# Performance work log

Hardware: AMD Instinct MI355X
Metric: run time of the kernel (lower is better)

## Reference

```python
import jax, jax.numpy as jnp
import numpy as np

T = 64        # n_estimators
DEPTH = 8
D = 2**DEPTH - 1   # internal nodes per tree (255)
K = 2**DEPTH       # leaves per tree (256)
M = 512       # n_features
C = 8         # class_num
B = 4096      # batch


def _build_path_masks():
    # Complete binary tree in heap order. For leaf l, walk from root;
    # going LEFT corresponds to b==+1 -> multiply (1 - x_node) -> Bpos,
    # going RIGHT corresponds to b==-1 -> multiply x_node -> Bneg.
    Bpos = np.zeros((K, D), dtype=np.float32)
    Bneg = np.zeros((K, D), dtype=np.float32)
    for l in range(K):
        node = 0
        for level in range(DEPTH):
            bit = (l >> (DEPTH - 1 - level)) & 1
            if bit == 0:
                Bpos[l, node] = 1.0
            else:
                Bneg[l, node] = 1.0
            node = 2 * node + 1 + bit
    return Bpos, Bneg


def setup_inputs() -> dict:
    rng = np.random.default_rng(0)
    key = jax.random.key(0)
    x = jax.random.normal(key, (B, M), dtype=jnp.float32)
    # fcn1: each internal node splits on one feature -> one-hot weight row,
    # bias = -threshold (change_parameters1).
    feat = rng.integers(0, M, size=(T, D))
    W1 = np.zeros((T, D, M), dtype=np.float32)
    W1[np.arange(T)[:, None], np.arange(D)[None, :], feat] = 1.0
    b1 = (-rng.standard_normal((T, D))).astype(np.float32)  # -threshold
    # Path masks shared across trees (complete trees), tiled per tree.
    Bpos1, Bneg1 = _build_path_masks()
    Bpos = np.broadcast_to(Bpos1, (T, K, D)).copy()
    Bneg = np.broadcast_to(Bneg1, (T, K, D)).copy()
    # fcn2 weight = c^T with zero bias (change_parameters2): leaf values [T, K, C]
    Cw = rng.random((T, K, C)).astype(np.float32)
    return {
        "input": x,
        "W1": jnp.asarray(W1),
        "b1": jnp.asarray(b1),
        "Bpos": jnp.asarray(Bpos),
        "Bneg": jnp.asarray(Bneg),
        "Cw": jnp.asarray(Cw),
    }


def reference(input, W1, b1, Bpos, Bneg, Cw):
    # z: [B, T, D] = 10 * (fcn1 per tree)
    z = 10.0 * (jnp.einsum("bm,tdm->btd", input, W1) + b1)
    # x = sigmoid(z); leaf-path product:
    #   x_c[b,t,k] = prod_d x^Bneg[t,k,d] * (1-x)^Bpos[t,k,d]
    # computed exactly in log-space (all factors in (0,1)):
    log_x = jax.nn.log_sigmoid(z)       # log sigmoid(z)
    log_1mx = jax.nn.log_sigmoid(-z)    # log (1 - sigmoid(z))
    log_xc = (jnp.einsum("btd,tkd->btk", log_x, Bneg)
              + jnp.einsum("btd,tkd->btk", log_1mx, Bpos))
    x_c = jnp.exp(log_xc)               # [B, T, K]
    # fcn2 (zero bias) then forest average over trees
    out = jnp.einsum("btk,tkc->bc", x_c, Cw) / T
    return out
```

## Files before the change

kernel.cpp:

```cpp
#include <hip/hip_runtime.h>
#include <hip/hip_bf16.h>

#define TT 64
#define DD 255
#define KK 256
#define MM 512
#define CC 8
#define BB 4096
#define NB 4

typedef _Float16 h2 __attribute__((ext_vector_type(2)));

__device__ __forceinline__ float wave_sum(float v) {
    v += __shfl_down(v, 32, 64);
    v += __shfl_down(v, 16, 64);
    v += __shfl_down(v, 8, 64);
    v += __shfl_down(v, 4, 64);
    v += __shfl_down(v, 2, 64);
    v += __shfl_down(v, 1, 64);
    return v;
}

__global__ void feat_kernel(const float* __restrict__ W1, int* __restrict__ feat) {
    const int row = blockIdx.x * 4 + (threadIdx.x >> 6);
    const int lane = threadIdx.x & 63;
    const float4* r = reinterpret_cast<const float4*>(W1 + (size_t)row * MM);
    float4 a = r[lane];
    float4 b = r[lane + 64];
    float ba = (float)(4 * lane);
    float bb = (float)(4 * (lane + 64));
    float acc = 0.0f;
    acc = fmaf(a.x, ba,        acc);
    acc = fmaf(a.y, ba + 1.0f, acc);
    acc = fmaf(a.z, ba + 2.0f, acc);
    acc = fmaf(a.w, ba + 3.0f, acc);
    acc = fmaf(b.x, bb,        acc);
    acc = fmaf(b.y, bb + 1.0f, acc);
    acc = fmaf(b.z, bb + 2.0f, acc);
    acc = fmaf(b.w, bb + 3.0f, acc);
    acc = wave_sum(acc);
    if (lane == 0) feat[row] = (int)(acc + 0.5f);
}

__device__ __forceinline__ float sigm_from(float xv, float c1) {
    float earg = fmaf(-14.426950408889634f, xv, c1);
    float e = exp2f(earg);
    return __builtin_amdgcn_rcpf(1.0f + e);
}

#define FMA4(acc, s, v)                         \
    do {                                        \
        (acc).x = fmaf((s), (v).x, (acc).x);    \
        (acc).y = fmaf((s), (v).y, (acc).y);    \
        (acc).z = fmaf((s), (v).z, (acc).z);    \
        (acc).w = fmaf((s), (v).w, (acc).w);    \
    } while (0)

__global__ __launch_bounds__(256, 4) void forest_kernel(
        const float* __restrict__ x, const float* __restrict__ b1,
        const float* __restrict__ Cw, const int* __restrict__ feat,
        float* __restrict__ out) {
    __shared__ float xsi[MM][NB];
    __shared__ h2 s8[NB * 2 * 256 * 2];
    __shared__ float4 red4[4][NB][2];

    const int tid = threadIdx.x;
    const int b0 = blockIdx.x * NB;

    for (int idx = tid; idx < MM * NB; idx += 256) {
        int m = idx & (MM - 1);
        int bl = idx >> 9;
        xsi[m][bl] = x[(size_t)(b0 + bl) * MM + m];
    }

    float4 accA[NB], accB[NB];
    #pragma unroll
    for (int bl = 0; bl < NB; ++bl) {
        accA[bl] = make_float4(0.f, 0.f, 0.f, 0.f);
        accB[bl] = make_float4(0.f, 0.f, 0.f, 0.f);
    }

    const int i = tid & 127;
    const int sub = tid >> 7;

    for (int g = 0; g < 8; ++g) {
        __syncthreads();
        if (tid < DD) {
            const int d = tid;
            int f[8];
            float c1[8];
            #pragma unroll
            for (int j = 0; j < 8; ++j) {
                int t = g * 8 + j;
                f[j] = feat[t * DD + d];
                c1[j] = -14.426950408889634f * b1[t * DD + d];
            }
            float sv[NB][8];
            #pragma unroll
            for (int j = 0; j < 8; ++j) {
                float4 xv = *reinterpret_cast<const float4*>(&xsi[f[j]][0]);
                sv[0][j] = sigm_from(xv.x, c1[j]);
                sv[1][j] = sigm_from(xv.y, c1[j]);
                sv[2][j] = sigm_from(xv.z, c1[j]);
                sv[3][j] = sigm_from(xv.w, c1[j]);
            }
            #pragma unroll
            for (int bl = 0; bl < NB; ++bl) {
                h2 p0 = {(_Float16)sv[bl][0], (_Float16)sv[bl][1]};
                h2 p1 = {(_Float16)sv[bl][2], (_Float16)sv[bl][3]};
                h2 p2 = {(_Float16)sv[bl][4], (_Float16)sv[bl][5]};
                h2 p3 = {(_Float16)sv[bl][6], (_Float16)sv[bl][7]};
                float2 w0, w1;
                w0.x = __builtin_bit_cast(float, p0);
                w0.y = __builtin_bit_cast(float, p1);
                w1.x = __builtin_bit_cast(float, p2);
                w1.y = __builtin_bit_cast(float, p3);
                *reinterpret_cast<float2*>(&s8[(bl * 2 + 0) * 512 + d * 2]) = w0;
                *reinterpret_cast<float2*>(&s8[(bl * 2 + 1) * 512 + d * 2]) = w1;
            }
        }
        __syncthreads();

        float4 cA0[4], cA1[4], cB0[4], cB1[4];
        #pragma unroll
        for (int j = 0; j < 4; ++j) {
            int t = g * 8 + sub * 4 + j;
            const float4* p = reinterpret_cast<const float4*>(
                Cw + ((size_t)t * KK + 2 * i) * CC);
            cA0[j] = p[0];
            cA1[j] = p[1];
            cB0[j] = p[2];
            cB1[j] = p[3];
        }

        h2 pre0[NB], pre1[NB];
        #pragma unroll
        for (int bl = 0; bl < NB; ++bl) {
            pre0[bl] = (h2){(_Float16)1.0f, (_Float16)1.0f};
            pre1[bl] = (h2){(_Float16)1.0f, (_Float16)1.0f};
        }

        #pragma unroll
        for (int lev = 0; lev < 7; ++lev) {
            int node = (1 << lev) - 1 + (i >> (7 - lev));
            int bit = (i >> (6 - lev)) & 1;
            _Float16 offs = (_Float16)(1 - bit);
            _Float16 sgs = (_Float16)(2 * bit - 1);
            h2 offv = {offs, offs};
            h2 sg = {sgs, sgs};
            #pragma unroll
            for (int bl = 0; bl < NB; ++bl) {
                float2 raw = *reinterpret_cast<const float2*>(
                    &s8[(bl * 2 + sub) * 512 + node * 2]);
                h2 s0 = __builtin_bit_cast(h2, raw.x);
                h2 s1 = __builtin_bit_cast(h2, raw.y);
                pre0[bl] *= (sg * s0 + offv);
                pre1[bl] *= (sg * s1 + offv);
            }
        }
        const int node7 = 127 + i;
        #pragma unroll
        for (int bl = 0; bl < NB; ++bl) {
            float2 raw = *reinterpret_cast<const float2*>(
                &s8[(bl * 2 + sub) * 512 + node7 * 2]);
            h2 s0 = __builtin_bit_cast(h2, raw.x);
            h2 s1 = __builtin_bit_cast(h2, raw.y);
            h2 one = {(_Float16)1.0f, (_Float16)1.0f};
            h2 pe0h = pre0[bl] * (one - s0);
            h2 po0h = pre0[bl] * s0;
            h2 pe1h = pre1[bl] * (one - s1);
            h2 po1h = pre1[bl] * s1;
            float pear[4] = {(float)pe0h.x, (float)pe0h.y,
                             (float)pe1h.x, (float)pe1h.y};
            float poar[4] = {(float)po0h.x, (float)po0h.y,
                             (float)po1h.x, (float)po1h.y};
            #pragma unroll
            for (int j = 0; j < 4; ++j) {
                FMA4(accA[bl], pear[j], cA0[j]);
                FMA4(accB[bl], pear[j], cA1[j]);
                FMA4(accA[bl], poar[j], cB0[j]);
                FMA4(accB[bl], poar[j], cB1[j]);
            }
        }
    }

    const int lane = tid & 63;
    const int wv = tid >> 6;
    #pragma unroll
    for (int bl = 0; bl < NB; ++bl) {
        accA[bl].x = wave_sum(accA[bl].x);
        accA[bl].y = wave_sum(accA[bl].y);
        accA[bl].z = wave_sum(accA[bl].z);
        accA[bl].w = wave_sum(accA[bl].w);
        accB[bl].x = wave_sum(accB[bl].x);
        accB[bl].y = wave_sum(accB[bl].y);
        accB[bl].z = wave_sum(accB[bl].z);
        accB[bl].w = wave_sum(accB[bl].w);
    }
    if (lane == 0) {
        #pragma unroll
        for (int bl = 0; bl < NB; ++bl) {
            red4[wv][bl][0] = accA[bl];
            red4[wv][bl][1] = accB[bl];
        }
    }
    __syncthreads();
    if (tid < NB * CC) {
        int bl = tid >> 3;
        int c = tid & 7;
        const float* r0 = reinterpret_cast<const float*>(&red4[0][bl][0]);
        const float* r1 = reinterpret_cast<const float*>(&red4[1][bl][0]);
        const float* r2 = reinterpret_cast<const float*>(&red4[2][bl][0]);
        const float* r3 = reinterpret_cast<const float*>(&red4[3][bl][0]);
        float s = r0[c] + r1[c] + r2[c] + r3[c];
        out[(size_t)(b0 + bl) * CC + c] = s * (1.0f / 64.0f);
    }
}

extern "C" void kernel_launch(void* const* d_in, const int* in_sizes, int n_in,
                              void* d_out, int out_size, void* d_ws, size_t ws_size,
                              hipStream_t stream) {
    const float* x  = (const float*)d_in[0];
    const float* W1 = (const float*)d_in[1];
    const float* b1 = (const float*)d_in[2];
    const float* Cw = (const float*)d_in[5];
    float* out = (float*)d_out;
    int* feat = (int*)d_ws;

    feat_kernel<<<(TT * DD) / 4, 256, 0, stream>>>(W1, feat);
    forest_kernel<<<BB / NB, 256, 0, stream>>>(x, b1, Cw, feat, out);
}
```

Baseline: 169.4 us.

## Use packed fp16 leaf accumulation and split trees across two grid halves

Replaces the fp32 FMA accumulation of leaf probability times class weight with packed half2 multiply-adds, converting Cw to fp16 in registers. The tree loop is split over a second grid dimension (two halves of 32 trees), and partial sums are combined with atomicAdd after a memset of the output. This roughly halves the ALU work of the reduction and doubles the block count for better occupancy. The cost is fp16 accumulation error, a duplicated x load per half, and atomics.

New measurement: 167.6 us. About the same (-1.0%).

```diff
diff --git a/kernel.cpp b/kernel.cpp
--- a/kernel.cpp
+++ b/kernel.cpp
@@ -8,6 +8,7 @@
 #define CC 8
 #define BB 4096
 #define NB 4
+#define TPB 32
 
 typedef _Float16 h2 __attribute__((ext_vector_type(2)));
 
@@ -48,24 +49,17 @@
     return __builtin_amdgcn_rcpf(1.0f + e);
 }
 
-#define FMA4(acc, s, v)                         \
-    do {                                        \
-        (acc).x = fmaf((s), (v).x, (acc).x);    \
-        (acc).y = fmaf((s), (v).y, (acc).y);    \
-        (acc).z = fmaf((s), (v).z, (acc).z);    \
-        (acc).w = fmaf((s), (v).w, (acc).w);    \
-    } while (0)
-
-__global__ __launch_bounds__(256, 4) void forest_kernel(
+__global__ __launch_bounds__(256, 2) void forest_kernel(
         const float* __restrict__ x, const float* __restrict__ b1,
         const float* __restrict__ Cw, const int* __restrict__ feat,
         float* __restrict__ out) {
     __shared__ float xsi[MM][NB];
     __shared__ h2 s8[NB * 2 * 256 * 2];
-    __shared__ float4 red4[4][NB][2];
+    __shared__ float red[4][NB][CC];
 
     const int tid = threadIdx.x;
     const int b0 = blockIdx.x * NB;
+    const int t0 = blockIdx.y * TPB;
 
     for (int idx = tid; idx < MM * NB; idx += 256) {
         int m = idx & (MM - 1);
@@ -73,17 +67,18 @@
         xsi[m][bl] = x[(size_t)(b0 + bl) * MM + m];
     }
 
-    float4 accA[NB], accB[NB];
+    h2 acc[NB][4];
     #pragma unroll
-    for (int bl = 0; bl < NB; ++bl) {
-        accA[bl] = make_float4(0.f, 0.f, 0.f, 0.f);
-        accB[bl] = make_float4(0.f, 0.f, 0.f, 0.f);
-    }
+    for (int bl = 0; bl < NB; ++bl)
+        #pragma unroll
+        for (int q = 0; q < 4; ++q)
+            acc[bl][q] = (h2){(_Float16)0.0f, (_Float16)0.0f};
 
     const int i = tid & 127;
     const int sub = tid >> 7;
-
-    for (int g = 0; g < 8; ++g) {
+    const h2 one = {(_Float16)1.0f, (_Float16)1.0f};
+
+    for (int g = 0; g < TPB / 8; ++g) {
         __syncthreads();
         if (tid < DD) {
             const int d = tid;
@@ -91,7 +86,7 @@
             float c1[8];
             #pragma unroll
             for (int j = 0; j < 8; ++j) {
-                int t = g * 8 + j;
+                int t = t0 + g * 8 + j;
                 f[j] = feat[t * DD + d];
                 c1[j] = -14.426950408889634f * b1[t * DD + d];
             }
@@ -121,23 +116,28 @@
         }
         __syncthreads();
 
-        float4 cA0[4], cA1[4], cB0[4], cB1[4];
+        h2 cwa[4][4], cwb[4][4];
         #pragma unroll
         for (int j = 0; j < 4; ++j) {
-            int t = g * 8 + sub * 4 + j;
+            int t = t0 + g * 8 + sub * 4 + j;
             const float4* p = reinterpret_cast<const float4*>(
                 Cw + ((size_t)t * KK + 2 * i) * CC);
-            cA0[j] = p[0];
-            cA1[j] = p[1];
-            cB0[j] = p[2];
-            cB1[j] = p[3];
+            float4 a0 = p[0], a1 = p[1], bv0 = p[2], bv1 = p[3];
+            cwa[j][0] = (h2){(_Float16)a0.x, (_Float16)a0.y};
+            cwa[j][1] = (h2){(_Float16)a0.z, (_Float16)a0.w};
+            cwa[j][2] = (h2){(_Float16)a1.x, (_Float16)a1.y};
+            cwa[j][3] = (h2){(_Float16)a1.z, (_Float16)a1.w};
+            cwb[j][0] = (h2){(_Float16)bv0.x, (_Float16)bv0.y};
+            cwb[j][1] = (h2){(_Float16)bv0.z, (_Float16)bv0.w};
+            cwb[j][2] = (h2){(_Float16)bv1.x, (_Float16)bv1.y};
+            cwb[j][3] = (h2){(_Float16)bv1.z, (_Float16)bv1.w};
         }
 
         h2 pre0[NB], pre1[NB];
         #pragma unroll
         for (int bl = 0; bl < NB; ++bl) {
-            pre0[bl] = (h2){(_Float16)1.0f, (_Float16)1.0f};
-            pre1[bl] = (h2){(_Float16)1.0f, (_Float16)1.0f};
+            pre0[bl] = one;
+            pre1[bl] = one;
         }
 
         #pragma unroll
@@ -165,55 +165,48 @@
                 &s8[(bl * 2 + sub) * 512 + node7 * 2]);
             h2 s0 = __builtin_bit_cast(h2, raw.x);
             h2 s1 = __builtin_bit_cast(h2, raw.y);
-            h2 one = {(_Float16)1.0f, (_Float16)1.0f};
-            h2 pe0h = pre0[bl] * (one - s0);
-            h2 po0h = pre0[bl] * s0;
-            h2 pe1h = pre1[bl] * (one - s1);
-            h2 po1h = pre1[bl] * s1;
-            float pear[4] = {(float)pe0h.x, (float)pe0h.y,
-                             (float)pe1h.x, (float)pe1h.y};
-            float poar[4] = {(float)po0h.x, (float)po0h.y,
-                             (float)po1h.x, (float)po1h.y};
-            #pragma unroll
-            for (int j = 0; j < 4; ++j) {
-                FMA4(accA[bl], pear[j], cA0[j]);
-                FMA4(accB[bl], pear[j], cA1[j]);
-                FMA4(accA[bl], poar[j], cB0[j]);
-                FMA4(accB[bl], poar[j], cB1[j]);
+            h2 pe0 = pre0[bl] * (one - s0);
+            h2 po0 = pre0[bl] * s0;
+            h2 pe1 = pre1[bl] * (one - s1);
+            h2 po1 = pre1[bl] * s1;
+            #pragma unroll
+            for (int q = 0; q < 4; ++q) {
+                acc[bl][q] += (h2){pe0.x, pe0.x} * cwa[0][q];
+                acc[bl][q] += (h2){po0.x, po0.x} * cwb[0][q];
+                acc[bl][q] += (h2){pe0.y, pe0.y} * cwa[1][q];
+                acc[bl][q] += (h2){po0.y, po0.y} * cwb[1][q];
+                acc[bl][q] += (h2){pe1.x, pe1.x} * cwa[2][q];
+                acc[bl][q] += (h2){po1.x, po1.x} * cwb[2][q];
+                acc[bl][q] += (h2){pe1.y, pe1.y} * cwa[3][q];
+                acc[bl][q] += (h2){po1.y, po1.y} * cwb[3][q];
             }
         }
     }
 
     const int lane = tid & 63;
     const int wv = tid >> 6;
+    float af[NB][CC];
     #pragma unroll
     for (int bl = 0; bl < NB; ++bl) {
-        accA[bl].x = wave_sum(accA[bl].x);
-        accA[bl].y = wave_sum(accA[bl].y);
-        accA[bl].z = wave_sum(accA[bl].z);
-        accA[bl].w = wave_sum(accA[bl].w);
-        accB[bl].x = wave_sum(accB[bl].x);
-        accB[bl].y = wave_sum(accB[bl].y);
-        accB[bl].z = wave_sum(accB[bl].z);
-        accB[bl].w = wave_sum(accB[bl].w);
+        #pragma unroll
+        for (int q = 0; q < 4; ++q) {
+            af[bl][2 * q]     = wave_sum((float)acc[bl][q].x);
+            af[bl][2 * q + 1] = wave_sum((float)acc[bl][q].y);
+        }
     }
     if (lane == 0) {
         #pragma unroll
-        for (int bl = 0; bl < NB; ++bl) {
-            red4[wv][bl][0] = accA[bl];
-            red4[wv][bl][1] = accB[bl];
-        }
+        for (int bl = 0; bl < NB; ++bl)
+            #pragma unroll
+            for (int c = 0; c < CC; ++c)
+                red[wv][bl][c] = af[bl][c];
     }
     __syncthreads();
     if (tid < NB * CC) {
         int bl = tid >> 3;
         int c = tid & 7;
-        const float* r0 = reinterpret_cast<const float*>(&red4[0][bl][0]);
-        const float* r1 = reinterpret_cast<const float*>(&red4[1][bl][0]);
-        const float* r2 = reinterpret_cast<const float*>(&red4[2][bl][0]);
-        const float* r3 = reinterpret_cast<const float*>(&red4[3][bl][0]);
-        float s = r0[c] + r1[c] + r2[c] + r3[c];
-        out[(size_t)(b0 + bl) * CC + c] = s * (1.0f / 64.0f);
+        float s = red[0][bl][c] + red[1][bl][c] + red[2][bl][c] + red[3][bl][c];
+        atomicAdd(&out[(size_t)(b0 + bl) * CC + c], s * (1.0f / 64.0f));
     }
 }
 
@@ -227,6 +220,7 @@
     float* out = (float*)d_out;
     int* feat = (int*)d_ws;
 
+    hipMemsetAsync(out, 0, (size_t)BB * CC * sizeof(float), stream);
     feat_kernel<<<(TT * DD) / 4, 256, 0, stream>>>(W1, feat);
-    forest_kernel<<<BB / NB, 256, 0, stream>>>(x, b1, Cw, feat, out);
-}
+    forest_kernel<<<dim3(BB / NB, 2), 256, 0, stream>>>(x, b1, Cw, feat, out);
+}
```
